# Optimization experiments

Measured on AMD Instinct MI355X. Metric: run time of the kernel, lower is better.

Reference implementation:

```python
import jax, jax.numpy as jnp
import numpy as np

# Dimensions: batch B, window W (time features), nodes M, hidden HID, hops NLAYERS
B, W, M, HID, NLAYERS = 32, 168, 2048, 128, 6


def setup_inputs() -> dict:
    key = jax.random.key(0)
    ks = jax.random.split(key, 6)
    x = jax.random.normal(ks[0], (B, W, M), dtype=jnp.float32)
    # scale L so matrix powers L^k stay bounded (spectral radius < 1)
    L = jax.random.normal(ks[1], (M, M), dtype=jnp.float32) / (2.0 * np.float32(np.sqrt(M)))
    # stacked per-hop MLP params: linears[i]: W->HID, linears2[i]: HID->1
    W1 = jax.random.normal(ks[2], (NLAYERS + 1, HID, W), dtype=jnp.float32) / np.float32(np.sqrt(W))
    b1 = jax.random.normal(ks[3], (NLAYERS + 1, HID), dtype=jnp.float32) * 0.01
    W2 = jax.random.normal(ks[4], (NLAYERS + 1, HID), dtype=jnp.float32) / np.float32(np.sqrt(HID))
    b2 = jax.random.normal(ks[5], (NLAYERS + 1,), dtype=jnp.float32) * 0.01
    return {"x": x, "L": L, "W1": W1, "b1": b1, "W2": W2, "b2": b2}


def _hop_mlp(t, w1, bb1, w2, bb2):
    # t: [B, M, W] -> scalar score per node: Linear(W->HID), ReLU, Linear(HID->1)
    h = jax.nn.relu(jnp.einsum('bmw,hw->bmh', t, w1) + bb1)
    return jnp.einsum('bmh,h->bm', h, w2) + bb2


def reference(x, L, W1, b1, W2, b2):
    xt = jnp.swapaxes(x, 1, 2)  # [B, M, W] (x.transpose(2,1))
    s = _hop_mlp(xt, W1[0], b1[0], W2[0], b2[0])  # [B, M]
    P = L
    for i in range(1, NLAYERS + 1):
        # PP.expand + bmm == broadcasted matmul; never materialize [B,M,M]
        t = jnp.einsum('ij,bjw->biw', P, xt)  # [B, M, W]
        s = s + _hop_mlp(t, W1[i], b1[i], W2[i], b2[i])
        P = jnp.matmul(L, P)  # next graph power
    return s  # [B, M]; output_fun is None so no final nonlinearity
```

## Files before the change

### kernel.cpp

```cpp
#include <hip/hip_runtime.h>
#include <cstdint>
#include <cstddef>

typedef __bf16 bf16_t;
typedef __attribute__((ext_vector_type(8))) __bf16 bf16x8;
typedef __attribute__((ext_vector_type(4))) __bf16 bf16x4;
typedef __attribute__((ext_vector_type(4))) float floatx4;

#define NB 32
#define NW 168
#define NM 2048
#define NHID 128
#define NBW (NB * NW)

#define GLOAD_LDS16(g, l)                                          \
  __builtin_amdgcn_global_load_lds(                                \
      (const __attribute__((address_space(1))) void*)(g),          \
      (__attribute__((address_space(3))) void*)(l), 16, 0, 0)

__global__ void cast_bf16_kernel(const float* __restrict__ in, bf16_t* __restrict__ out, int n4) {
  int stride = gridDim.x * blockDim.x;
  for (int i = blockIdx.x * blockDim.x + threadIdx.x; i < n4; i += stride) {
    float4 v = ((const float4*)in)[i];
    bf16x4 o = {(bf16_t)v.x, (bf16_t)v.y, (bf16_t)v.z, (bf16_t)v.w};
    ((bf16x4*)out)[i] = o;
  }
}

__global__ void prep_x_kernel(const float* __restrict__ x, bf16_t* __restrict__ Xb,
                              bf16_t* __restrict__ XT) {
  __shared__ float tile[64][65];
  const int R = NBW, C = NM;
  int r0 = blockIdx.y * 64, c0 = blockIdx.x * 64;
  int t = threadIdx.x;
  int tr = t >> 4, tc4 = (t & 15) * 4;
#pragma unroll
  for (int p = 0; p < 4; ++p) {
    int row = p * 16 + tr;
    float4 v = *(const float4*)(x + (size_t)(r0 + row) * C + c0 + tc4);
    tile[row][tc4 + 0] = v.x;
    tile[row][tc4 + 1] = v.y;
    tile[row][tc4 + 2] = v.z;
    tile[row][tc4 + 3] = v.w;
    bf16x4 o = {(bf16_t)v.x, (bf16_t)v.y, (bf16_t)v.z, (bf16_t)v.w};
    *(bf16x4*)(Xb + (size_t)(r0 + row) * C + c0 + tc4) = o;
  }
  __syncthreads();
#pragma unroll
  for (int p = 0; p < 4; ++p) {
    int c = p * 16 + tr;
    bf16x4 o = {(bf16_t)tile[tc4 + 0][c], (bf16_t)tile[tc4 + 1][c],
                (bf16_t)tile[tc4 + 2][c], (bf16_t)tile[tc4 + 3][c]};
    *(bf16x4*)(XT + (size_t)(c0 + c) * R + r0 + tc4) = o;
  }
}

#define STAGE2(gbase, ld, t, ks, ldsbase)                                        \
  do {                                                                           \
    const bf16_t* _g = (gbase) + (size_t)(t) * 64 + (ks) * 32;                   \
    GLOAD_LDS16(_g, lds + (ldsbase) + (ks) * 8192 + wv * 512);                   \
    GLOAD_LDS16(_g + (size_t)128 * (ld),                                         \
                lds + (ldsbase) + (ks) * 8192 + 4096 + wv * 512);                \
  } while (0)

#define VM4 asm volatile("s_waitcnt vmcnt(4)" ::: "memory")

#define PHASE(bufoff, ks, mh, READB, STG, WAIT)                                  \
  do {                                                                           \
    if (READB) {                                                                 \
      _Pragma("unroll") for (int ni = 0; ni < 4; ++ni)                           \
          bfr[ni] = *(const bf16x8*)(pB + (bufoff) + (ks) * 8192 + ni * 512);    \
    }                                                                            \
    _Pragma("unroll") for (int mi = 0; mi < 4; ++mi)                             \
        afr[mi] =                                                                \
            *(const bf16x8*)(pA + (bufoff) + (ks) * 8192 + ((mh) * 4 + mi) * 512); \
    STG;                                                                         \
    WAIT;                                                                        \
    __builtin_amdgcn_s_barrier();                                                \
    asm volatile("s_waitcnt lgkmcnt(0)" ::: "memory");                           \
    __builtin_amdgcn_sched_barrier(0);                                           \
    __builtin_amdgcn_s_setprio(1);                                               \
    _Pragma("unroll") for (int mi = 0; mi < 4; ++mi)                             \
        _Pragma("unroll") for (int ni = 0; ni < 4; ++ni)                         \
            acc[(mh) * 4 + mi][ni] = __builtin_amdgcn_mfma_f32_16x16x32_bf16(    \
                afr[mi], bfr[ni], acc[(mh) * 4 + mi][ni], 0, 0, 0);              \
    __builtin_amdgcn_s_setprio(0);                                               \
    __builtin_amdgcn_s_barrier();                                                \
  } while (0)

__global__ __launch_bounds__(512, 2) void gemm_nt_kernel(
    const bf16_t* __restrict__ A, const bf16_t* __restrict__ Bt,
    bf16_t* __restrict__ C, bf16_t* __restrict__ Ct,
    int K, int lda, int ldb, int ldc, int ldct, int write_c) {
  __shared__ bf16_t lds[65536];
  const int tid = threadIdx.x;
  const int m0 = blockIdx.y * 256, n0 = blockIdx.x * 256;
  const int lane = tid & 63, wv = tid >> 6;
  const int wm = wv >> 2, wn = wv & 3;
  const int quad = lane >> 4, l15 = lane & 15;

  const int srow = tid >> 2;
  const int scsw = (tid & 3) ^ (srow & 3);
  const bf16_t* aS = A + (size_t)(m0 + srow) * lda + scsw * 8;
  const bf16_t* bS = Bt + (size_t)(n0 + srow) * ldb + scsw * 8;

  const int fsw = (quad ^ (l15 & 3)) * 8;
  const bf16_t* pA = lds + (size_t)(wm * 128 + l15) * 32 + fsw;
  const bf16_t* pB = lds + 16384 + (size_t)(wn * 64 + l15) * 32 + fsw;

  floatx4 zero4 = {0.f, 0.f, 0.f, 0.f};
  floatx4 acc[8][4];
#pragma unroll
  for (int mi = 0; mi < 8; ++mi)
#pragma unroll
    for (int ni = 0; ni < 4; ++ni) acc[mi][ni] = zero4;

  STAGE2(aS, lda, 0, 0, 0);
  STAGE2(bS, ldb, 0, 0, 16384);
  STAGE2(aS, lda, 0, 1, 0);
  STAGE2(bS, ldb, 0, 1, 16384);
  STAGE2(aS, lda, 1, 0, 32768);
  STAGE2(bS, ldb, 1, 0, 49152);
  VM4;
  __builtin_amdgcn_s_barrier();

  bf16x8 afr[4], bfr[4];
  const int nt = K >> 6;
  const int nit = K >> 7;
#pragma unroll 1
  for (int i = 0; i < nit; ++i) {
    const int t1 = 2 * i + 1;
    const int t2 = (t1 + 1 < nt) ? t1 + 1 : 0;
    const int t3 = (t1 + 2 < nt) ? t1 + 2 : 0;
    PHASE(0,     0, 0, 1, STAGE2(aS, lda, t1, 1, 32768), (void)0);
    PHASE(0,     0, 1, 0, STAGE2(bS, ldb, t1, 1, 49152), (void)0);
    PHASE(0,     1, 0, 1, STAGE2(aS, lda, t2, 0, 0),     (void)0);
    PHASE(0,     1, 1, 0, STAGE2(bS, ldb, t2, 0, 16384), VM4);
    PHASE(32768, 0, 0, 1, STAGE2(aS, lda, t2, 1, 0),     (void)0);
    PHASE(32768, 0, 1, 0, STAGE2(bS, ldb, t2, 1, 16384), (void)0);
    PHASE(32768, 1, 0, 1, STAGE2(aS, lda, t3, 0, 32768), (void)0);
    PHASE(32768, 1, 1, 0, STAGE2(bS, ldb, t3, 0, 49152), VM4);
  }
  asm volatile("s_waitcnt vmcnt(0)" ::: "memory");

#pragma unroll
  for (int mi = 0; mi < 8; ++mi) {
#pragma unroll
    for (int ni = 0; ni < 4; ++ni) {
      int col = n0 + wn * 64 + ni * 16 + l15;
      int rowb = m0 + wm * 128 + mi * 16 + quad * 4;
      bf16x4 tv;
#pragma unroll
      for (int r = 0; r < 4; ++r) tv[r] = (bf16_t)acc[mi][ni][r];
      *(bf16x4*)(Ct + (size_t)col * ldct + rowb) = tv;
      if (write_c) {
#pragma unroll
        for (int r = 0; r < 4; ++r)
          C[(size_t)(rowb + r) * ldc + col] = tv[r];
      }
    }
  }
}

__global__ void mlp_score_kernel(const bf16_t* __restrict__ T, const bf16_t* __restrict__ W1b,
                                 const float* __restrict__ b1, const float* __restrict__ W2,
                                 const float* __restrict__ b2, float* __restrict__ out,
                                 int hop, int accumulate) {
  __shared__ bf16_t Bs[24 * 128 * 8];
  __shared__ float sred[4][64];
  const bf16_t* Wh = W1b + (size_t)hop * NHID * NW;
  const float* b1h = b1 + hop * NHID;
  const float* w2h = W2 + hop * NHID;
  int tid = threadIdx.x;
  int r0 = blockIdx.x * 128;
  int lane = tid & 63, wv = tid >> 6;
  int wm = wv >> 1, wn = wv & 1;
  int quad = lane >> 4, l15 = lane & 15;

  for (int c = 2688 + tid; c < 3072; c += 256) {
    int4 z = {0, 0, 0, 0};
    *(int4*)(Bs + (size_t)c * 8) = z;
  }
  for (int i = 0; i < 11; ++i) {
    int c = i * 256 + tid;
    if (c < 2688) {
      int kc = c >> 7;
      int h = (c & 127) ^ ((kc & 3) << 2);
      GLOAD_LDS16(Wh + (size_t)h * NW + kc * 8, Bs + (size_t)(i * 256 + wv * 64) * 8);
    }
  }

  const bf16_t* arow[4];
#pragma unroll
  for (int mi = 0; mi < 4; ++mi) {
    int R = r0 + wm * 64 + mi * 16 + l15;
    arow[mi] = T + (size_t)(R >> 5) * NBW + (size_t)(R & 31) * NW + quad * 8;
  }

  floatx4 zero4 = {0.f, 0.f, 0.f, 0.f};
  floatx4 acc[4][4];
#pragma unroll
  for (int mi = 0; mi < 4; ++mi)
#pragma unroll
    for (int ni = 0; ni < 4; ++ni) acc[mi][ni] = zero4;

  __syncthreads();

#pragma unroll
  for (int kb = 0; kb < 192; kb += 32) {
    int kc = (kb >> 3) + quad;
    bf16x8 af[4], bf[4];
#pragma unroll
    for (int mi = 0; mi < 4; ++mi)
      af[mi] = *(const bf16x8*)(arow[mi] + kb);
#pragma unroll
    for (int ni = 0; ni < 4; ++ni) {
      int hpos = (wn * 64 + ni * 16 + l15) ^ ((kc & 3) << 2);
      bf[ni] = *(const bf16x8*)(Bs + (size_t)(kc * 128 + hpos) * 8);
    }
#pragma unroll
    for (int mi = 0; mi < 4; ++mi)
#pragma unroll
      for (int ni = 0; ni < 4; ++ni)
        acc[mi][ni] = __builtin_amdgcn_mfma_f32_16x16x32_bf16(af[mi], bf[ni], acc[mi][ni], 0, 0, 0);
  }

  float part[4][4];
#pragma unroll
  for (int mi = 0; mi < 4; ++mi)
#pragma unroll
    for (int r = 0; r < 4; ++r) part[mi][r] = 0.f;
#pragma unroll
  for (int ni = 0; ni < 4; ++ni) {
    int col = wn * 64 + ni * 16 + l15;
    float b1v = b1h[col];
    float w2v = w2h[col];
#pragma unroll
    for (int mi = 0; mi < 4; ++mi)
#pragma unroll
      for (int r = 0; r < 4; ++r) {
        float h = acc[mi][ni][r] + b1v;
        h = h > 0.f ? h : 0.f;
        part[mi][r] += h * w2v;
      }
  }
#pragma unroll
  for (int off = 1; off < 16; off <<= 1)
#pragma unroll
    for (int mi = 0; mi < 4; ++mi)
#pragma unroll
      for (int r = 0; r < 4; ++r) part[mi][r] += __shfl_xor(part[mi][r], off);
  if (l15 == 0) {
#pragma unroll
    for (int mi = 0; mi < 4; ++mi)
#pragma unroll
      for (int r = 0; r < 4; ++r) sred[wv][mi * 16 + quad * 4 + r] = part[mi][r];
  }
  __syncthreads();
  if (tid < 128) {
    int half = tid >> 6;
    int lr = tid & 63;
    float v = sred[half * 2][lr] + sred[half * 2 + 1][lr] + b2[hop];
    int R = r0 + half * 64 + lr;
    int idx = (R & 31) * NM + (R >> 5);
    if (accumulate)
      out[idx] += v;
    else
      out[idx] = v;
  }
}

extern "C" void kernel_launch(void* const* d_in, const int* in_sizes, int n_in,
                              void* d_out, int out_size, void* d_ws, size_t ws_size,
                              hipStream_t stream) {
  const float* x = (const float*)d_in[0];
  const float* L = (const float*)d_in[1];
  const float* W1 = (const float*)d_in[2];
  const float* b1 = (const float*)d_in[3];
  const float* W2 = (const float*)d_in[4];
  const float* b2 = (const float*)d_in[5];
  float* out = (float*)d_out;

  char* ws = (char*)d_ws;
  size_t off = 0;
  auto walloc = [&](size_t bytes) -> void* {
    off = (off + 255) & ~(size_t)255;
    void* p = ws + off;
    off += bytes;
    return p;
  };
  bf16_t* Xb = (bf16_t*)walloc((size_t)NBW * NM * 2);
  bf16_t* XT = (bf16_t*)walloc((size_t)NM * NBW * 2);
  bf16_t* Lb = (bf16_t*)walloc((size_t)NM * NM * 2);
  bf16_t* W1b = (bf16_t*)walloc((size_t)7 * NHID * NW * 2);
  bf16_t* Ta = (bf16_t*)walloc((size_t)NBW * NM * 2);
  (void)ws_size; (void)in_sizes; (void)n_in; (void)out_size;

  prep_x_kernel<<<dim3(NM / 64, NBW / 64), dim3(256), 0, stream>>>(x, Xb, XT);
  cast_bf16_kernel<<<dim3(1024), dim3(256), 0, stream>>>(L, Lb, NM * NM / 4);
  cast_bf16_kernel<<<dim3(64), dim3(256), 0, stream>>>(W1, W1b, 7 * NHID * NW / 4);

  mlp_score_kernel<<<dim3(NM * NB / 128), dim3(256), 0, stream>>>(XT, W1b, b1, W2, b2, out, 0, 0);

  bf16_t* src = Xb;
  bf16_t* dst = Ta;
  for (int i = 1; i <= 6; ++i) {
    gemm_nt_kernel<<<dim3(NM / 256, NBW / 256), dim3(512), 0, stream>>>(
        src, Lb, dst, XT, NM, NM, NM, NM, NBW, (i < 6) ? 1 : 0);
    mlp_score_kernel<<<dim3(NM * NB / 128), dim3(256), 0, stream>>>(XT, W1b, b1, W2, b2, out, i, 1);
    bf16_t* t = src; src = dst; dst = t;
  }
}
```

Baseline: 571.4 us.

## Overlap each hop's MLP scoring with the next propagation GEMM in one launch

Merges the GEMM for hop i and the MLP scoring for hop i-1 into a single launch. Extra blocks past the GEMM tiles run two MLP halves each, reading a double-buffered transposed activation, so the MLP work overlaps GEMM execution and fills idle CUs. Only the final hop's MLP runs as a separate launch. The GEMM's LDS swizzle pattern also changes to reduce bank conflicts. In exchange it needs a second XT buffer, and the mixed grid may unbalance the block schedule.

```diff
diff --git a/kernel.cpp b/kernel.cpp
--- a/kernel.cpp
+++ b/kernel.cpp
@@ -12,6 +12,8 @@
 #define NM 2048
 #define NHID 128
 #define NBW (NB * NW)
+#define NGEMM 168
+#define NMLPB 256
 
 #define GLOAD_LDS16(g, l)                                          \
   __builtin_amdgcn_global_load_lds(                                \
@@ -52,6 +54,108 @@
     bf16x4 o = {(bf16_t)tile[tc4 + 0][c], (bf16_t)tile[tc4 + 1][c],
                 (bf16_t)tile[tc4 + 2][c], (bf16_t)tile[tc4 + 3][c]};
     *(bf16x4*)(XT + (size_t)(c0 + c) * R + r0 + tc4) = o;
+  }
+}
+
+__device__ __forceinline__ void mlp_half(
+    int t2, int r0, bf16_t* __restrict__ Bs, float* __restrict__ sred,
+    const bf16_t* __restrict__ T, const bf16_t* __restrict__ Wh,
+    const float* __restrict__ b1h, const float* __restrict__ w2h, float b2v,
+    float* __restrict__ out, int accumulate) {
+  int lane = t2 & 63, wvh = t2 >> 6;
+  int wm = wvh >> 1, wn = wvh & 1;
+  int quad = lane >> 4, l15 = lane & 15;
+
+  for (int c = 2688 + t2; c < 3072; c += 256) {
+    int4 z = {0, 0, 0, 0};
+    *(int4*)(Bs + (size_t)c * 8) = z;
+  }
+  for (int i = 0; i < 11; ++i) {
+    int c = i * 256 + t2;
+    if (c < 2688) {
+      int kc = c >> 7;
+      int h = (c & 127) ^ ((kc & 3) << 2);
+      GLOAD_LDS16(Wh + (size_t)h * NW + kc * 8, Bs + (size_t)(i * 256 + wvh * 64) * 8);
+    }
+  }
+
+  const bf16_t* arow[4];
+#pragma unroll
+  for (int mi = 0; mi < 4; ++mi) {
+    int R = r0 + wm * 64 + mi * 16 + l15;
+    arow[mi] = T + (size_t)(R >> 5) * NBW + (size_t)(R & 31) * NW + quad * 8;
+  }
+
+  floatx4 zero4 = {0.f, 0.f, 0.f, 0.f};
+  floatx4 acc[4][4];
+#pragma unroll
+  for (int mi = 0; mi < 4; ++mi)
+#pragma unroll
+    for (int ni = 0; ni < 4; ++ni) acc[mi][ni] = zero4;
+
+  __syncthreads();
+
+#pragma unroll
+  for (int kb = 0; kb < 192; kb += 32) {
+    int kc = (kb >> 3) + quad;
+    bf16x8 af[4], bf[4];
+#pragma unroll
+    for (int mi = 0; mi < 4; ++mi)
+      af[mi] = *(const bf16x8*)(arow[mi] + kb);
+#pragma unroll
+    for (int ni = 0; ni < 4; ++ni) {
+      int hpos = (wn * 64 + ni * 16 + l15) ^ ((kc & 3) << 2);
+      bf[ni] = *(const bf16x8*)(Bs + (size_t)(kc * 128 + hpos) * 8);
+    }
+#pragma unroll
+    for (int mi = 0; mi < 4; ++mi)
+#pragma unroll
+      for (int ni = 0; ni < 4; ++ni)
+        acc[mi][ni] = __builtin_amdgcn_mfma_f32_16x16x32_bf16(af[mi], bf[ni], acc[mi][ni], 0, 0, 0);
+  }
+
+  float part[4][4];
+#pragma unroll
+  for (int mi = 0; mi < 4; ++mi)
+#pragma unroll
+    for (int r = 0; r < 4; ++r) part[mi][r] = 0.f;
+#pragma unroll
+  for (int ni = 0; ni < 4; ++ni) {
+    int col = wn * 64 + ni * 16 + l15;
+    float b1v = b1h[col];
+    float w2v = w2h[col];
+#pragma unroll
+    for (int mi = 0; mi < 4; ++mi)
+#pragma unroll
+      for (int r = 0; r < 4; ++r) {
+        float h = acc[mi][ni][r] + b1v;
+        h = h > 0.f ? h : 0.f;
+        part[mi][r] += h * w2v;
+      }
+  }
+#pragma unroll
+  for (int off = 1; off < 16; off <<= 1)
+#pragma unroll
+    for (int mi = 0; mi < 4; ++mi)
+#pragma unroll
+      for (int r = 0; r < 4; ++r) part[mi][r] += __shfl_xor(part[mi][r], off);
+  if (l15 == 0) {
+#pragma unroll
+    for (int mi = 0; mi < 4; ++mi)
+#pragma unroll
+      for (int r = 0; r < 4; ++r) sred[wvh * 64 + mi * 16 + quad * 4 + r] = part[mi][r];
+  }
+  __syncthreads();
+  if (t2 < 128) {
+    int hh = t2 >> 6;
+    int lr = t2 & 63;
+    float v = sred[(hh * 2) * 64 + lr] + sred[(hh * 2 + 1) * 64 + lr] + b2v;
+    int R = r0 + hh * 64 + lr;
+    int idx = (R & 31) * NM + (R >> 5);
+    if (accumulate)
+      out[idx] += v;
+    else
+      out[idx] = v;
   }
 }
 
@@ -88,23 +192,41 @@
     __builtin_amdgcn_s_barrier();                                                \
   } while (0)
 
-__global__ __launch_bounds__(512, 2) void gemm_nt_kernel(
+__global__ __launch_bounds__(512, 2) void fused_gemm_mlp_kernel(
     const bf16_t* __restrict__ A, const bf16_t* __restrict__ Bt,
     bf16_t* __restrict__ C, bf16_t* __restrict__ Ct,
-    int K, int lda, int ldb, int ldc, int ldct, int write_c) {
+    int K, int lda, int ldb, int ldc, int ldct, int write_c,
+    const bf16_t* __restrict__ T, const bf16_t* __restrict__ W1b,
+    const float* __restrict__ b1, const float* __restrict__ W2,
+    const float* __restrict__ b2, float* __restrict__ out,
+    int hop, int accumulate) {
   __shared__ bf16_t lds[65536];
+  const int bx = blockIdx.x;
   const int tid = threadIdx.x;
-  const int m0 = blockIdx.y * 256, n0 = blockIdx.x * 256;
+
+  if (bx >= NGEMM) {
+    int j = bx - NGEMM;
+    int h = tid >> 8;
+    int t2 = tid & 255;
+    bf16_t* Bs = lds + (size_t)h * 24576;
+    float* sred = (float*)(lds + 49152) + h * 256;
+    int r0 = (2 * j + h) * 128;
+    mlp_half(t2, r0, Bs, sred, T, W1b + (size_t)hop * NHID * NW,
+             b1 + hop * NHID, W2 + hop * NHID, b2[hop], out, accumulate);
+    return;
+  }
+
+  const int m0 = (bx >> 3) * 256, n0 = (bx & 7) * 256;
   const int lane = tid & 63, wv = tid >> 6;
   const int wm = wv >> 2, wn = wv & 3;
   const int quad = lane >> 4, l15 = lane & 15;
 
   const int srow = tid >> 2;
-  const int scsw = (tid & 3) ^ (srow & 3);
+  const int scsw = (tid & 3) ^ ((srow >> 1) & 3);
   const bf16_t* aS = A + (size_t)(m0 + srow) * lda + scsw * 8;
   const bf16_t* bS = Bt + (size_t)(n0 + srow) * ldb + scsw * 8;
 
-  const int fsw = (quad ^ (l15 & 3)) * 8;
+  const int fsw = (quad ^ ((l15 >> 1) & 3)) * 8;
   const bf16_t* pA = lds + (size_t)(wm * 128 + l15) * 32 + fsw;
   const bf16_t* pB = lds + 16384 + (size_t)(wn * 64 + l15) * 32 + fsw;
 
@@ -167,107 +289,10 @@
                                  const float* __restrict__ b2, float* __restrict__ out,
                                  int hop, int accumulate) {
   __shared__ bf16_t Bs[24 * 128 * 8];
-  __shared__ float sred[4][64];
-  const bf16_t* Wh = W1b + (size_t)hop * NHID * NW;
-  const float* b1h = b1 + hop * NHID;
-  const float* w2h = W2 + hop * NHID;
-  int tid = threadIdx.x;
-  int r0 = blockIdx.x * 128;
-  int lane = tid & 63, wv = tid >> 6;
-  int wm = wv >> 1, wn = wv & 1;
-  int quad = lane >> 4, l15 = lane & 15;
-
-  for (int c = 2688 + tid; c < 3072; c += 256) {
-    int4 z = {0, 0, 0, 0};
-    *(int4*)(Bs + (size_t)c * 8) = z;
-  }
-  for (int i = 0; i < 11; ++i) {
-    int c = i * 256 + tid;
-    if (c < 2688) {
-      int kc = c >> 7;
-      int h = (c & 127) ^ ((kc & 3) << 2);
-      GLOAD_LDS16(Wh + (size_t)h * NW + kc * 8, Bs + (size_t)(i * 256 + wv * 64) * 8);
-    }
-  }
-
-  const bf16_t* arow[4];
-#pragma unroll
-  for (int mi = 0; mi < 4; ++mi) {
-    int R = r0 + wm * 64 + mi * 16 + l15;
-    arow[mi] = T + (size_t)(R >> 5) * NBW + (size_t)(R & 31) * NW + quad * 8;
-  }
-
-  floatx4 zero4 = {0.f, 0.f, 0.f, 0.f};
-  floatx4 acc[4][4];
-#pragma unroll
-  for (int mi = 0; mi < 4; ++mi)
-#pragma unroll
-    for (int ni = 0; ni < 4; ++ni) acc[mi][ni] = zero4;
-
-  __syncthreads();
-
-#pragma unroll
-  for (int kb = 0; kb < 192; kb += 32) {
-    int kc = (kb >> 3) + quad;
-    bf16x8 af[4], bf[4];
-#pragma unroll
-    for (int mi = 0; mi < 4; ++mi)
-      af[mi] = *(const bf16x8*)(arow[mi] + kb);
-#pragma unroll
-    for (int ni = 0; ni < 4; ++ni) {
-      int hpos = (wn * 64 + ni * 16 + l15) ^ ((kc & 3) << 2);
-      bf[ni] = *(const bf16x8*)(Bs + (size_t)(kc * 128 + hpos) * 8);
-    }
-#pragma unroll
-    for (int mi = 0; mi < 4; ++mi)
-#pragma unroll
-      for (int ni = 0; ni < 4; ++ni)
-        acc[mi][ni] = __builtin_amdgcn_mfma_f32_16x16x32_bf16(af[mi], bf[ni], acc[mi][ni], 0, 0, 0);
-  }
-
-  float part[4][4];
-#pragma unroll
-  for (int mi = 0; mi < 4; ++mi)
-#pragma unroll
-    for (int r = 0; r < 4; ++r) part[mi][r] = 0.f;
-#pragma unroll
-  for (int ni = 0; ni < 4; ++ni) {
-    int col = wn * 64 + ni * 16 + l15;
-    float b1v = b1h[col];
-    float w2v = w2h[col];
-#pragma unroll
-    for (int mi = 0; mi < 4; ++mi)
-#pragma unroll
-      for (int r = 0; r < 4; ++r) {
-        float h = acc[mi][ni][r] + b1v;
-        h = h > 0.f ? h : 0.f;
-        part[mi][r] += h * w2v;
-      }
-  }
-#pragma unroll
-  for (int off = 1; off < 16; off <<= 1)
-#pragma unroll
-    for (int mi = 0; mi < 4; ++mi)
-#pragma unroll
-      for (int r = 0; r < 4; ++r) part[mi][r] += __shfl_xor(part[mi][r], off);
-  if (l15 == 0) {
-#pragma unroll
-    for (int mi = 0; mi < 4; ++mi)
-#pragma unroll
-      for (int r = 0; r < 4; ++r) sred[wv][mi * 16 + quad * 4 + r] = part[mi][r];
-  }
-  __syncthreads();
-  if (tid < 128) {
-    int half = tid >> 6;
-    int lr = tid & 63;
-    float v = sred[half * 2][lr] + sred[half * 2 + 1][lr] + b2[hop];
-    int R = r0 + half * 64 + lr;
-    int idx = (R & 31) * NM + (R >> 5);
-    if (accumulate)
-      out[idx] += v;
-    else
-      out[idx] = v;
-  }
+  __shared__ float sred[256];
+  mlp_half(threadIdx.x, blockIdx.x * 128, Bs, sred, T,
+           W1b + (size_t)hop * NHID * NW, b1 + hop * NHID, W2 + hop * NHID,
+           b2[hop], out, accumulate);
 }
 
 extern "C" void kernel_launch(void* const* d_in, const int* in_sizes, int n_in,
@@ -290,24 +315,28 @@
     return p;
   };
   bf16_t* Xb = (bf16_t*)walloc((size_t)NBW * NM * 2);
-  bf16_t* XT = (bf16_t*)walloc((size_t)NM * NBW * 2);
+  bf16_t* XT0 = (bf16_t*)walloc((size_t)NM * NBW * 2);
+  bf16_t* XT1 = (bf16_t*)walloc((size_t)NM * NBW * 2);
   bf16_t* Lb = (bf16_t*)walloc((size_t)NM * NM * 2);
   bf16_t* W1b = (bf16_t*)walloc((size_t)7 * NHID * NW * 2);
   bf16_t* Ta = (bf16_t*)walloc((size_t)NBW * NM * 2);
   (void)ws_size; (void)in_sizes; (void)n_in; (void)out_size;
 
-  prep_x_kernel<<<dim3(NM / 64, NBW / 64), dim3(256), 0, stream>>>(x, Xb, XT);
+  prep_x_kernel<<<dim3(NM / 64, NBW / 64), dim3(256), 0, stream>>>(x, Xb, XT0);
   cast_bf16_kernel<<<dim3(1024), dim3(256), 0, stream>>>(L, Lb, NM * NM / 4);
   cast_bf16_kernel<<<dim3(64), dim3(256), 0, stream>>>(W1, W1b, 7 * NHID * NW / 4);
 
-  mlp_score_kernel<<<dim3(NM * NB / 128), dim3(256), 0, stream>>>(XT, W1b, b1, W2, b2, out, 0, 0);
-
   bf16_t* src = Xb;
   bf16_t* dst = Ta;
+  bf16_t* xtprev = XT0;
+  bf16_t* xtcur = XT1;
   for (int i = 1; i <= 6; ++i) {
-    gemm_nt_kernel<<<dim3(NM / 256, NBW / 256), dim3(512), 0, stream>>>(
-        src, Lb, dst, XT, NM, NM, NM, NM, NBW, (i < 6) ? 1 : 0);
-    mlp_score_kernel<<<dim3(NM * NB / 128), dim3(256), 0, stream>>>(XT, W1b, b1, W2, b2, out, i, 1);
+    fused_gemm_mlp_kernel<<<dim3(NGEMM + NMLPB), dim3(512), 0, stream>>>(
+        src, Lb, dst, xtcur, NM, NM, NM, NM, NBW, (i < 6) ? 1 : 0,
+        xtprev, W1b, b1, W2, b2, out, i - 1, (i > 1) ? 1 : 0);
     bf16_t* t = src; src = dst; dst = t;
-  }
-}
+    t = xtprev; xtprev = xtcur; xtcur = t;
+  }
+  mlp_score_kernel<<<dim3(NM * NB / 128), dim3(256), 0, stream>>>(
+      xtprev, W1b, b1, W2, b2, out, 6, 1);
+}
```

New measurement: 482.4 us. 15.6% less time.
